# Kernel tuning notes

Hardware: AMD Instinct MI355X
Metric: run time of the kernel (lower is better)

## Reference

```python
import jax, jax.numpy as jnp
import numpy as np
from jax import lax

N = 16384      # total nodes (NG graphs x PER nodes)
PER = 512      # nodes per graph
NG = 32        # number of graphs
E = 262144     # edges (avg degree 16)
NEG = jnp.float32(-1e30)


def gcn_conv(x, W, b, src, dst, em, n):
    # PyG GCNConv: h = xW; add *remaining* self-loops; symmetric norm; aggregate at dst; + bias
    h = x @ W
    w = em.astype(x.dtype)
    selfw = jax.ops.segment_sum(jnp.where((src == dst) & em, 1.0, 0.0), dst, num_segments=n)
    has_self = (selfw > 0).astype(x.dtype)
    deg = jax.ops.segment_sum(w, dst, num_segments=n) + (1.0 - has_self)
    dinv = lax.rsqrt(deg)
    norm = dinv[src] * dinv[dst] * w                      # [E]
    agg = jax.ops.segment_sum(norm[:, None] * h[src], dst, num_segments=n)
    return agg + ((1.0 - has_self) / deg)[:, None] * h + b


def edge_pool(x, src, dst, em, nvalid, Pw, Pb, n):
    # PyG EdgePooling with softmax edge scores, add_to_edge_score=0.1, eval-mode dropout (identity)
    e = src.shape[0]
    raw = (jnp.concatenate([x[src], x[dst]], axis=1) @ Pw)[:, 0] + Pb[0]
    # softmax over edges grouped by target node
    logits = jnp.where(em, raw, NEG)
    mx = jax.ops.segment_max(logits, dst, num_segments=n)
    ex = jnp.where(em, jnp.exp(raw - mx[dst]), 0.0)
    den = jax.ops.segment_sum(ex, dst, num_segments=n)
    score = jnp.where(em, ex / jnp.maximum(den[dst], 1e-16), 0.0) + 0.1
    # greedy sequential edge contraction in descending score order (matches PyG __merge_edges__)
    key = lax.stop_gradient(jnp.where(em, score, NEG))
    order = jnp.argsort(-key)

    def step(marked, sdm):
        s, d, mk = sdm
        ok = mk & ~marked[s] & ~marked[d]
        m1 = marked.at[s].set(marked[s] | ok)
        m2 = m1.at[d].set(m1[d] | ok)
        return m2, ok

    _, ch_sorted = lax.scan(step, ~nvalid, (src[order], dst[order], em[order]))
    chosen = jnp.zeros(e, bool).at[order].set(ch_sorted)

    rep = jnp.minimum(src, dst)
    oth = jnp.maximum(src, dst)
    SEN = n  # out-of-range index -> dropped scatter
    cluster = jnp.arange(n, dtype=src.dtype).at[jnp.where(chosen, oth, SEN)].set(rep, mode='drop')
    node_score = jnp.ones(n, x.dtype).at[jnp.where(chosen, rep, SEN)].set(score, mode='drop')
    absorbed = jnp.zeros(n, bool).at[jnp.where(chosen & (src != dst), oth, SEN)].set(True, mode='drop')
    new_valid = nvalid & ~absorbed
    # new_x[c] = (sum of x over cluster) * edge score (1 for unmatched nodes)
    new_x = jax.ops.segment_sum(x, cluster, num_segments=n) * node_score[:, None]
    new_x = new_x * new_valid[:, None].astype(x.dtype)
    # remap + coalesce edges (dedupe); padding kept via mask
    ns, nd = cluster[src], cluster[dst]
    ekey = jnp.where(em, ns * n + nd, n * n)
    eo = jnp.argsort(ekey)
    ks = ekey[eo]
    dup = jnp.concatenate([jnp.zeros(1, bool), ks[1:] == ks[:-1]])
    return new_x, ns[eo], nd[eo], (ks < n * n) & ~dup, new_valid


def _forward(x, W1, b1, W2, b2, W3, b3, P1w, P1b, P2w, P2b, P3w, P3b,
             L1w, L1b, L2w, L2b, L3w, L3b, edge_index, batch):
    n = x.shape[0]
    src, dst = edge_index[0], edge_index[1]
    em = jnp.ones(src.shape[0], bool)
    nv = jnp.ones(n, bool)
    h = gcn_conv(x, W1, b1, src, dst, em, n)
    h, src, dst, em, nv = edge_pool(h, src, dst, em, nv, P1w, P1b, n)
    h = jax.nn.relu(h)
    h = gcn_conv(h, W2, b2, src, dst, em, n)
    h, src, dst, em, nv = edge_pool(h, src, dst, em, nv, P2w, P2b, n)
    h = jax.nn.relu(h)
    h = gcn_conv(h, W3, b3, src, dst, em, n)
    h, src, dst, em, nv = edge_pool(h, src, dst, em, nv, P3w, P3b, n)
    h = jax.nn.relu(h)
    beff = jnp.where(nv, batch, NG)                       # invalid nodes -> dummy segment
    g = jax.ops.segment_max(h, beff, num_segments=NG + 1)[:NG]
    z = jax.nn.relu(g @ L1w + L1b)
    z = jax.nn.relu(z @ L2w + L2b)
    z = jax.nn.relu(z @ L3w + L3b)
    return jax.nn.softmax(z, axis=-1)


def _lin(k, fi, fo):
    w = jax.random.normal(k, (fi, fo), jnp.float32) * (1.0 / np.sqrt(fi))
    return w, jnp.zeros((fo,), jnp.float32)


def setup_inputs() -> dict:
    key = jax.random.key(0)
    ks = jax.random.split(key, 16)
    x = jax.random.normal(ks[0], (N, 107), jnp.float32)
    src = jax.random.randint(ks[1], (E,), 0, N, dtype=jnp.int32)
    dst = (src // PER) * PER + jax.random.randint(ks[2], (E,), 0, PER, dtype=jnp.int32)
    edge_index = jnp.stack([src, dst])
    batch = jnp.arange(N, dtype=jnp.int32) // PER
    W1, b1 = _lin(ks[3], 107, 200)
    W2, b2 = _lin(ks[4], 200, 400)
    W3, b3 = _lin(ks[5], 400, 600)
    P1w, P1b = _lin(ks[6], 400, 1)
    P2w, P2b = _lin(ks[7], 800, 1)
    P3w, P3b = _lin(ks[8], 1200, 1)
    L1w, L1b = _lin(ks[9], 600, 200)
    L2w, L2b = _lin(ks[10], 200, 20)
    L3w, L3b = _lin(ks[11], 20, 4)
    return dict(x=x, edge_index=edge_index, batch=batch,
                W1=W1, b1=b1, W2=W2, b2=b2, W3=W3, b3=b3,
                P1w=P1w, P1b=P1b, P2w=P2w, P2b=P2b, P3w=P3w, P3b=P3b,
                L1w=L1w, L1b=L1b, L2w=L2w, L2b=L2b, L3w=L3w, L3b=L3b)


def reference(x, edge_index, batch, W1, b1, W2, b2, W3, b3,
              P1w, P1b, P2w, P2b, P3w, P3b, L1w, L1b, L2w, L2b, L3w, L3b):
    return _forward(x, W1, b1, W2, b2, W3, b3, P1w, P1b, P2w, P2b, P3w, P3b,
                    L1w, L1b, L2w, L2b, L3w, L3b, edge_index, batch)
```

## Files before the change

kernel.cpp:

```cpp
#include <hip/hip_runtime.h>

#define NN 16384
#define PERG 512
#define NGR 32
#define NE 262144
#define GSEG 9216

__device__ __forceinline__ unsigned encf(float f){
  unsigned u = __float_as_uint(f);
  return (u & 0x80000000u) ? ~u : (u | 0x80000000u);
}
__device__ __forceinline__ float decf(unsigned e){
  unsigned u = (e & 0x80000000u) ? (e ^ 0x80000000u) : ~e;
  return __uint_as_float(u);
}

__global__ void k_padx(const float* __restrict__ x, float* __restrict__ xp){
  int i = blockIdx.x*256 + threadIdx.x;
  if (i < NN*112){ int r = i/112, c = i-r*112; xp[i] = (c<107) ? x[r*107+c] : 0.f; }
}
__global__ void k_padw(const float* __restrict__ Wsrc, float* __restrict__ Wdst,
                       int Ksrc, int Kdst, int N){
  int i = blockIdx.x*256 + threadIdx.x;
  if (i < Kdst*N){ int r = i/N, c = i-r*N; Wdst[i] = (r<Ksrc) ? Wsrc[r*N+c] : 0.f; }
}

__global__ __launch_bounds__(256) void k_bucket(const int* __restrict__ ei, int* __restrict__ gcount,
    int* __restrict__ bsrc, int* __restrict__ bdst, int* __restrict__ bem, int* __restrict__ beid){
  __shared__ int cnt[NGR];
  __shared__ int base[NGR];
  int t = threadIdx.x;
  if (t < NGR) cnt[t] = 0;
  __syncthreads();
  int e = blockIdx.x*256 + t;
  int s=0,d=0,g=0,r=0;
  bool ok = (e < NE);
  if (ok){ s = ei[e]; d = ei[NE+e]; g = s >> 9; r = atomicAdd(&cnt[g],1); }
  __syncthreads();
  if (t < NGR) base[t] = atomicAdd(&gcount[t], cnt[t]);
  __syncthreads();
  if (ok){
    int pos = g*GSEG + base[g] + r;
    bsrc[pos]=s; bdst[pos]=d; bem[pos]=1; beid[pos]=e;
  }
}
__global__ void k_init_nodes(int* __restrict__ valid){
  int i = blockIdx.x*256 + threadIdx.x;
  if (i < NN) valid[i]=1;
}

__global__ __launch_bounds__(256) void k_mm(const float* __restrict__ A, const float* __restrict__ W,
                                            float* __restrict__ C, int KP, int N){
  __shared__ float As[16][132];
  __shared__ float Ws[16][68];
  int col0 = blockIdx.x*64, row0 = blockIdx.y*128;
  int t = threadIdx.x;
  int tx = t & 15, ty = t >> 4;
  int ar = t >> 1;
  int ak = (t & 1) * 8;
  int wk = t >> 4;
  int wn = (t & 15) * 4;
  int wc = col0 + wn;

  float acc[8][4];
#pragma unroll
  for (int i=0;i<8;i++)
#pragma unroll
    for (int j=0;j<4;j++) acc[i][j]=0.f;

  const float* Arow = A + (size_t)(row0+ar)*KP;

  for (int k0=0; k0<KP; k0+=16){
    float4 a0 = *(const float4*)&Arow[k0 + ak];
    float4 a1 = *(const float4*)&Arow[k0 + ak + 4];
    float4 w0;
    const float* wp = &W[(size_t)(k0+wk)*N + wc];
    if (wc+3 < N) w0 = *(const float4*)wp;
    else { w0.x=(wc<N)?wp[0]:0.f; w0.y=(wc+1<N)?wp[1]:0.f; w0.z=(wc+2<N)?wp[2]:0.f; w0.w=0.f; }
    __syncthreads();
    As[ak+0][ar]=a0.x; As[ak+1][ar]=a0.y; As[ak+2][ar]=a0.z; As[ak+3][ar]=a0.w;
    As[ak+4][ar]=a1.x; As[ak+5][ar]=a1.y; As[ak+6][ar]=a1.z; As[ak+7][ar]=a1.w;
    *(float4*)&Ws[wk][wn] = w0;
    __syncthreads();
#pragma unroll
    for (int kk=0;kk<16;kk++){
      float4 A0 = *(const float4*)&As[kk][ty*8];
      float4 A1 = *(const float4*)&As[kk][ty*8+4];
      float4 B0 = *(const float4*)&Ws[kk][tx*4];
      float a[8] = {A0.x,A0.y,A0.z,A0.w,A1.x,A1.y,A1.z,A1.w};
      float b[4] = {B0.x,B0.y,B0.z,B0.w};
#pragma unroll
      for (int i=0;i<8;i++)
#pragma unroll
        for (int j=0;j<4;j++) acc[i][j] += a[i]*b[j];
    }
  }

#pragma unroll
  for (int i=0;i<8;i++){
    int r = row0 + ty*8 + i;
    int cc = col0 + tx*4;
    if (cc+3 < N){
      float4 v = {acc[i][0],acc[i][1],acc[i][2],acc[i][3]};
      *(float4*)&C[(size_t)r*N+cc] = v;
    } else {
#pragma unroll
      for (int j=0;j<4;j++) if (cc+j<N) C[(size_t)r*N+cc+j] = acc[i][j];
    }
  }
}

__global__ __launch_bounds__(1024) void k_prep(const int* __restrict__ bsrc, const int* __restrict__ bdst,
    const int* __restrict__ bem, const int* __restrict__ gcount,
    int* __restrict__ row_s, int* __restrict__ row_e, int* __restrict__ elist,
    float* __restrict__ dinv, float* __restrict__ selfco){
  int g = blockIdx.x, t = threadIdx.x;
  __shared__ int cnt_l[PERG];
  __shared__ int scn[PERG];
  __shared__ int cur[PERG];
  __shared__ unsigned char hs_l[PERG];
  if (t<PERG){ cnt_l[t]=0; hs_l[t]=0; }
  __syncthreads();
  int nE = min(gcount[g], GSEG); int base = g*GSEG;
  for (int k=t;k<nE;k+=1024){
    if (bem[base+k]){
      int d = bdst[base+k]&511;
      atomicAdd(&cnt_l[d],1);
      if (bsrc[base+k]==bdst[base+k]) hs_l[d]=1;
    }
  }
  __syncthreads();
  if (t<PERG) scn[t]=cnt_l[t];
  __syncthreads();
  for (int off=1; off<PERG; off<<=1){
    int v = (t<PERG && t>=off) ? scn[t-off] : 0;
    __syncthreads();
    if (t<PERG) scn[t]+=v;
    __syncthreads();
  }
  if (t<PERG){
    int excl = scn[t]-cnt_l[t];
    row_s[g*PERG+t] = base+excl;
    row_e[g*PERG+t] = base+scn[t];
    cur[t] = excl;
    float deg = (float)cnt_l[t] + (hs_l[t]?0.f:1.f);
    dinv[g*PERG+t]   = rsqrtf(deg);
    selfco[g*PERG+t] = hs_l[t]?0.f:(1.f/deg);
  }
  __syncthreads();
  for (int k=t;k<nE;k+=1024){
    if (bem[base+k]){
      int d = bdst[base+k]&511;
      elist[base + atomicAdd(&cur[d],1)] = base+k;
    }
  }
}

template<int FO>
__global__ __launch_bounds__(256) void k_aggab(const float* __restrict__ h, const int* __restrict__ row_s,
    const int* __restrict__ row_e, const int* __restrict__ elist, const int* __restrict__ bsrc,
    const float* __restrict__ dinv, const float* __restrict__ selfco, const float* __restrict__ bias,
    const float* __restrict__ Pw, float* __restrict__ y, float* __restrict__ aval, float* __restrict__ bval){
  constexpr int Q = (FO+63)/64;
  int lane = threadIdx.x & 63;
  int nblk = (blockIdx.x & 7)*512 + (blockIdx.x >> 3);
  int i = nblk*4 + (threadIdx.x>>6);
  float acc[Q];
#pragma unroll
  for (int q=0;q<Q;q++) acc[q]=0.f;
  int s0 = row_s[i], s1 = row_e[i];
  float di = dinv[i];
  for (int p=s0; p<s1; p++){
    int e = elist[p]; int s = bsrc[e];
    float nr = di * dinv[s];
    const float* hrow = h + (size_t)s*FO;
#pragma unroll
    for (int q=0;q<Q;q++){ int c=lane+q*64; if (c<FO) acc[q] += nr*hrow[c]; }
  }
  float sc = selfco[i];
  const float* hi = h + (size_t)i*FO;
  float* yi = y + (size_t)i*FO;
  float sa=0.f, sb=0.f;
#pragma unroll
  for (int q=0;q<Q;q++){
    int c = lane+q*64;
    if (c<FO){
      float v = acc[q] + sc*hi[c] + bias[c];
      yi[c] = v;
      sa += v*Pw[c];
      sb += v*Pw[FO+c];
    }
  }
  for (int o=32;o;o>>=1){ sa += __shfl_xor(sa,o); sb += __shfl_xor(sb,o); }
  if (lane==0){ aval[i]=sa; bval[i]=sb; }
}

#define NEPT 9
__global__ __launch_bounds__(1024) void k_pool(const int* __restrict__ gcount,
    int* __restrict__ bsrc, int* __restrict__ bdst, int* __restrict__ bem, const int* __restrict__ beid,
    const float* __restrict__ aval, const float* __restrict__ bval, const float* __restrict__ Pb,
    float* __restrict__ nscore, int* __restrict__ partner, int* __restrict__ valid, int* __restrict__ table){
  int g = blockIdx.x, t = threadIdx.x;
  __shared__ unsigned mx[PERG];
  __shared__ float den[PERG];
  __shared__ unsigned long long best[PERG];
  __shared__ unsigned char marked[PERG];
  __shared__ unsigned short clus[PERG];
  __shared__ int flag;
  int nE = min(gcount[g], GSEG), base = g*GSEG;
  if (t<PERG){
    mx[t]=0u; den[t]=0.f;
    marked[t] = valid[g*PERG+t] ? 0 : 1;
    clus[t] = (unsigned short)t;
    nscore[g*PERG+t] = 1.f;
    partner[g*PERG+t] = -1;
  }
  __syncthreads();

  int sL[NEPT], dL[NEPT];
  float rawv[NEPT];
  unsigned em = 0u;
#pragma unroll
  for (int j=0;j<NEPT;j++){
    sL[j]=0; dL[j]=0; rawv[j]=0.f;
    int k = t + j*1024;
    if (k < nE && bem[base+k]){
      sL[j] = bsrc[base+k]&511; dL[j] = bdst[base+k]&511;
      rawv[j] = aval[(g<<9)+sL[j]] + bval[(g<<9)+dL[j]] + Pb[0];
      em |= (1u<<j);
      atomicMax(&mx[dL[j]], encf(rawv[j]));
    }
  }
  __syncthreads();
  float exv[NEPT];
#pragma unroll
  for (int j=0;j<NEPT;j++){
    exv[j]=0.f;
    if (em & (1u<<j)){
      exv[j] = expf(rawv[j] - decf(mx[dL[j]]));
      atomicAdd(&den[dL[j]], exv[j]);
    }
  }
  __syncthreads();
  unsigned long long pri[NEPT];
#pragma unroll
  for (int j=0;j<NEPT;j++){
    pri[j]=0ull;
    if (em & (1u<<j)){
      int k = t + j*1024;
      float sc = exv[j]/fmaxf(den[dL[j]],1e-16f) + 0.1f;
      pri[j] = ((unsigned long long)__float_as_uint(sc) << 18)
             | (unsigned long long)(0x3FFFFu - (unsigned)beid[base+k]);
    }
  }

  unsigned live = em;
  for (int round=0; round<512; ++round){
    if (t<PERG) best[t]=0ull;
    if (t==0) flag = 0;
    __syncthreads();
    int any = 0;
#pragma unroll
    for (int j=0;j<NEPT;j++){
      if (!(live & (1u<<j))) continue;
      int ls=sL[j], ld=dL[j];
      if (marked[ls] | marked[ld]){ live &= ~(1u<<j); continue; }
      any = 1;
      atomicMax(&best[ls], pri[j]);
      if (ld != ls) atomicMax(&best[ld], pri[j]);
    }
    if (any) flag = 1;
    __syncthreads();
    if (!flag) break;
#pragma unroll
    for (int j=0;j<NEPT;j++){
      if (!(live & (1u<<j))) continue;
      int ls=sL[j], ld=dL[j];
      unsigned long long p = pri[j];
      if (best[ls]==p && best[ld]==p){
        int repl = min(ls,ld), oth = max(ls,ld);
        clus[oth] = (unsigned short)repl;
        nscore[g*PERG+repl] = __uint_as_float((unsigned)(p>>18));
        if (ls != ld){ valid[g*PERG+oth] = 0; partner[g*PERG+repl] = g*PERG+oth; }
        marked[ls] = 1; marked[ld] = 1;
        live &= ~(1u<<j);
      }
    }
    __syncthreads();
  }
  __syncthreads();

#pragma unroll
  for (int j=0;j<NEPT;j++){
    if (em & (1u<<j)){
      int k = t + j*1024;
      int ns = clus[sL[j]], nd = clus[dL[j]];
      sL[j]=ns; dL[j]=nd;
      bsrc[base+k] = (g<<9)+ns; bdst[base+k] = (g<<9)+nd;
      table[(g<<18) | (ns<<9) | nd] = 0x7FFFFFFF;
    }
  }
  __syncthreads();
#pragma unroll
  for (int j=0;j<NEPT;j++){
    if (em & (1u<<j)){
      int k = t + j*1024;
      atomicMin(&table[(g<<18) | (sL[j]<<9) | dL[j]], base+k);
    }
  }
  __syncthreads();
#pragma unroll
  for (int j=0;j<NEPT;j++){
    if (em & (1u<<j)){
      int k = t + j*1024;
      if (table[(g<<18) | (sL[j]<<9) | dL[j]] != base+k) bem[base+k] = 0;
    }
  }
}

template<int FO, int FOP>
__global__ __launch_bounds__(256) void k_newx(const float* __restrict__ y, const int* __restrict__ partner,
    const float* __restrict__ nscore, const int* __restrict__ valid, float* __restrict__ out){
  constexpr int Q = (FOP+63)/64;
  int lane = threadIdx.x & 63;
  int nblk = (blockIdx.x & 7)*512 + (blockIdx.x >> 3);
  int i = nblk*4 + (threadIdx.x>>6);
  int v = valid[i];
  float ns = nscore[i];
  int p = partner[i];
  const float* yi = y + (size_t)i*FO;
  const float* yp = (p>=0) ? (y + (size_t)p*FO) : yi;
  float* oi = out + (size_t)i*FOP;
#pragma unroll
  for (int q=0;q<Q;q++){
    int c = lane + q*64;
    if (c<FO){
      float val = yi[c];
      if (p>=0) val += yp[c];
      val *= ns;
      oi[c] = v ? fmaxf(val,0.f) : 0.f;
    } else if (c<FOP){
      oi[c] = 0.f;
    }
  }
}

__global__ __launch_bounds__(256) void k_gmax(const float* __restrict__ x, const int* __restrict__ valid,
                                              float* __restrict__ part){
  int g = blockIdx.x >> 3, rp = blockIdx.x & 7;
  __shared__ int lv[64];
  int r0 = rp*64;
  if (threadIdx.x < 64) lv[threadIdx.x] = valid[g*PERG + r0 + threadIdx.x];
  __syncthreads();
  const float* base = x + ((size_t)g*PERG + r0)*600;
  for (int c=threadIdx.x; c<600; c+=256){
    float m = -1e30f;
    for (int r=0;r<64;r++)
      if (lv[r]) m = fmaxf(m, base[(size_t)r*600+c]);
    part[(size_t)(g*8+rp)*600 + c] = m;
  }
}
__global__ __launch_bounds__(256) void k_head(const float* __restrict__ part,
    const float* __restrict__ L1w, const float* __restrict__ L1b,
    const float* __restrict__ L2w, const float* __restrict__ L2b,
    const float* __restrict__ L3w, const float* __restrict__ L3b, float* __restrict__ out){
  int g = blockIdx.x, t = threadIdx.x;
  __shared__ float gg[600];
  __shared__ float z1[200];
  __shared__ float z2[20];
  __shared__ float z3[4];
  for (int c=t;c<600;c+=256){
    float m = -1e30f;
#pragma unroll
    for (int rp=0;rp<8;rp++) m = fmaxf(m, part[(size_t)(g*8+rp)*600 + c]);
    gg[c] = m;
  }
  __syncthreads();
  if (t<200){
    float s = L1b[t];
#pragma unroll 4
    for (int k=0;k<600;k++) s += gg[k]*L1w[k*200+t];
    z1[t] = fmaxf(s,0.f);
  }
  __syncthreads();
  if (t<20){
    float s = L2b[t];
#pragma unroll 4
    for (int k=0;k<200;k++) s += z1[k]*L2w[k*20+t];
    z2[t] = fmaxf(s,0.f);
  }
  __syncthreads();
  if (t<4){
    float s = L3b[t];
    for (int k=0;k<20;k++) s += z2[k]*L3w[k*4+t];
    z3[t] = fmaxf(s,0.f);
  }
  __syncthreads();
  if (t==0){
    float m = fmaxf(fmaxf(z3[0],z3[1]), fmaxf(z3[2],z3[3]));
    float e0=expf(z3[0]-m), e1=expf(z3[1]-m), e2=expf(z3[2]-m), e3=expf(z3[3]-m);
    float s = e0+e1+e2+e3;
    out[g*4+0]=e0/s; out[g*4+1]=e1/s; out[g*4+2]=e2/s; out[g*4+3]=e3/s;
  }
}

struct WsPtrs {
  float *A, *B, *x0p, *W1p, *W2p;
  int *bsrc, *bdst, *bem, *beid;
  int *elist, *row_s, *row_e;
  float *dinv, *selfco, *aval, *bval;
  float *nscore; int *partner; int *valid;
  int *gcount;
  float *gbuf;
};

extern "C" void kernel_launch(void* const* d_in, const int* in_sizes, int n_in,
                              void* d_out, int out_size, void* d_ws, size_t ws_size,
                              hipStream_t stream){
  const float* x0  = (const float*)d_in[0];
  const int*   ei  = (const int*)  d_in[1];
  const float* W1  = (const float*)d_in[3];  const float* b1  = (const float*)d_in[4];
  const float* W2  = (const float*)d_in[5];  const float* b2  = (const float*)d_in[6];
  const float* W3  = (const float*)d_in[7];  const float* b3  = (const float*)d_in[8];
  const float* P1w = (const float*)d_in[9];  const float* P1b = (const float*)d_in[10];
  const float* P2w = (const float*)d_in[11]; const float* P2b = (const float*)d_in[12];
  const float* P3w = (const float*)d_in[13]; const float* P3b = (const float*)d_in[14];
  const float* L1w = (const float*)d_in[15]; const float* L1b = (const float*)d_in[16];
  const float* L2w = (const float*)d_in[17]; const float* L2b = (const float*)d_in[18];
  const float* L3w = (const float*)d_in[19]; const float* L3b = (const float*)d_in[20];
  float* out = (float*)d_out;

  char* w = (char*)d_ws;
  size_t off = 0;
  auto alloc = [&](size_t bytes)->void*{
    void* p = w + off;
    off += bytes;
    off = (off + 255) & ~(size_t)255;
    return p;
  };
  WsPtrs P;
  P.A     = (float*)alloc((size_t)NN*600*4);
  P.B     = (float*)alloc((size_t)NN*600*4);
  P.x0p   = (float*)alloc((size_t)NN*112*4);
  P.W1p   = (float*)alloc((size_t)112*200*4);
  P.W2p   = (float*)alloc((size_t)208*400*4);
  P.bsrc  = (int*)  alloc((size_t)NGR*GSEG*4);
  P.bdst  = (int*)  alloc((size_t)NGR*GSEG*4);
  P.bem   = (int*)  alloc((size_t)NGR*GSEG*4);
  P.beid  = (int*)  alloc((size_t)NGR*GSEG*4);
  P.elist = (int*)  alloc((size_t)NGR*GSEG*4);
  P.row_s = (int*)  alloc((size_t)NN*4);
  P.row_e = (int*)  alloc((size_t)NN*4);
  P.dinv   = (float*)alloc((size_t)NN*4);
  P.selfco = (float*)alloc((size_t)NN*4);
  P.aval   = (float*)alloc((size_t)NN*4);
  P.bval   = (float*)alloc((size_t)NN*4);
  P.nscore = (float*)alloc((size_t)NN*4);
  P.partner= (int*)  alloc((size_t)NN*4);
  P.valid  = (int*)  alloc((size_t)NN*4);
  P.gcount = (int*)  alloc((size_t)NGR*4);
  P.gbuf   = (float*)alloc((size_t)NGR*8*600*4);
  (void)ws_size; (void)in_sizes; (void)n_in; (void)out_size;

  const int NG4 = NN/4;

  k_padx<<<(NN*112+255)/256,256,0,stream>>>(x0, P.x0p);
  k_padw<<<(112*200+255)/256,256,0,stream>>>(W1, P.W1p, 107, 112, 200);
  k_padw<<<(208*400+255)/256,256,0,stream>>>(W2, P.W2p, 200, 208, 400);
  hipMemsetAsync(P.gcount, 0, NGR*sizeof(int), stream);
  k_bucket<<<NE/256,256,0,stream>>>(ei, P.gcount, P.bsrc, P.bdst, P.bem, P.beid);
  k_init_nodes<<<NN/256,256,0,stream>>>(P.valid);

  { dim3 gmm(4,128); k_mm<<<gmm,256,0,stream>>>(P.x0p, P.W1p, P.A, 112, 200); }
  k_prep<<<NGR,1024,0,stream>>>(P.bsrc,P.bdst,P.bem,P.gcount,P.row_s,P.row_e,P.elist,P.dinv,P.selfco);
  k_aggab<200><<<NG4,256,0,stream>>>(P.A,P.row_s,P.row_e,P.elist,P.bsrc,P.dinv,P.selfco,b1,P1w,P.B,P.aval,P.bval);
  k_pool<<<NGR,1024,0,stream>>>(P.gcount,P.bsrc,P.bdst,P.bem,P.beid,P.aval,P.bval,P1b,
                                P.nscore,P.partner,P.valid,(int*)P.A);
  k_newx<200,208><<<NG4,256,0,stream>>>(P.B,P.partner,P.nscore,P.valid,P.A);

  { dim3 gmm(7,128); k_mm<<<gmm,256,0,stream>>>(P.A, P.W2p, P.B, 208, 400); }
  k_prep<<<NGR,1024,0,stream>>>(P.bsrc,P.bdst,P.bem,P.gcount,P.row_s,P.row_e,P.elist,P.dinv,P.selfco);
  k_aggab<400><<<NG4,256,0,stream>>>(P.B,P.row_s,P.row_e,P.elist,P.bsrc,P.dinv,P.selfco,b2,P2w,P.A,P.aval,P.bval);
  k_pool<<<NGR,1024,0,stream>>>(P.gcount,P.bsrc,P.bdst,P.bem,P.beid,P.aval,P.bval,P2b,
                                P.nscore,P.partner,P.valid,(int*)P.B);
  k_newx<400,400><<<NG4,256,0,stream>>>(P.A,P.partner,P.nscore,P.valid,P.B);

  { dim3 gmm(10,128); k_mm<<<gmm,256,0,stream>>>(P.B, W3, P.A, 400, 600); }
  k_prep<<<NGR,1024,0,stream>>>(P.bsrc,P.bdst,P.bem,P.gcount,P.row_s,P.row_e,P.elist,P.dinv,P.selfco);
  k_aggab<600><<<NG4,256,0,stream>>>(P.A,P.row_s,P.row_e,P.elist,P.bsrc,P.dinv,P.selfco,b3,P3w,P.B,P.aval,P.bval);
  k_pool<<<NGR,1024,0,stream>>>(P.gcount,P.bsrc,P.bdst,P.bem,P.beid,P.aval,P.bval,P3b,
                                P.nscore,P.partner,P.valid,(int*)P.A);
  k_newx<600,600><<<NG4,256,0,stream>>>(P.B,P.partner,P.nscore,P.valid,P.A);

  k_gmax<<<NGR*8,256,0,stream>>>(P.A, P.valid, P.gbuf);
  k_head<<<NGR,256,0,stream>>>(P.gbuf, L1w, L1b, L2w, L2b, L3w, L3b, out);
}
```

Baseline: 988.2 us.

## Replace edge-parallel greedy matching rounds with node-centric incidence-list scans

Builds a per-graph node incidence CSR (both endpoints) in k_prep and rewrites the k_pool matching loop so each unmarked node scans its incident edges for the best unmarked neighbour, instead of every edge doing 64-bit atomicMax on shared per-node best values each round. Scores go into shared memory and ties are broken by loading edge ids from global memory. This removes shared atomics and the wide priority keys, but it adds a second prefix scan and CSR build in k_prep. It also uses only 512 of 1024 threads per round with serial per-node loops, and raises the round cap to 600.

```diff
diff --git a/kernel.cpp b/kernel.cpp
--- a/kernel.cpp
+++ b/kernel.cpp
@@ -113,20 +113,25 @@
 __global__ __launch_bounds__(1024) void k_prep(const int* __restrict__ bsrc, const int* __restrict__ bdst,
     const int* __restrict__ bem, const int* __restrict__ gcount,
     int* __restrict__ row_s, int* __restrict__ row_e, int* __restrict__ elist,
+    int* __restrict__ inc, int* __restrict__ inc_rs, int* __restrict__ inc_re,
     float* __restrict__ dinv, float* __restrict__ selfco){
   int g = blockIdx.x, t = threadIdx.x;
   __shared__ int cnt_l[PERG];
+  __shared__ int cnt2[PERG];
   __shared__ int scn[PERG];
   __shared__ int cur[PERG];
+  __shared__ int cur2[PERG];
   __shared__ unsigned char hs_l[PERG];
-  if (t<PERG){ cnt_l[t]=0; hs_l[t]=0; }
-  __syncthreads();
-  int nE = min(gcount[g], GSEG); int base = g*GSEG;
+  if (t<PERG){ cnt_l[t]=0; cnt2[t]=0; hs_l[t]=0; }
+  __syncthreads();
+  int nE = min(gcount[g], GSEG); int base = g*GSEG; int base2 = g*2*GSEG;
   for (int k=t;k<nE;k+=1024){
     if (bem[base+k]){
-      int d = bdst[base+k]&511;
+      int d = bdst[base+k]&511, s = bsrc[base+k]&511;
       atomicAdd(&cnt_l[d],1);
-      if (bsrc[base+k]==bdst[base+k]) hs_l[d]=1;
+      if (s==d) hs_l[d]=1;
+      atomicAdd(&cnt2[d],1);
+      atomicAdd(&cnt2[s],1);
     }
   }
   __syncthreads();
@@ -148,10 +153,27 @@
     selfco[g*PERG+t] = hs_l[t]?0.f:(1.f/deg);
   }
   __syncthreads();
+  if (t<PERG) scn[t]=cnt2[t];
+  __syncthreads();
+  for (int off=1; off<PERG; off<<=1){
+    int v = (t<PERG && t>=off) ? scn[t-off] : 0;
+    __syncthreads();
+    if (t<PERG) scn[t]+=v;
+    __syncthreads();
+  }
+  if (t<PERG){
+    int excl = scn[t]-cnt2[t];
+    inc_rs[g*PERG+t] = base2+excl;
+    inc_re[g*PERG+t] = base2+scn[t];
+    cur2[t] = excl;
+  }
+  __syncthreads();
   for (int k=t;k<nE;k+=1024){
     if (bem[base+k]){
-      int d = bdst[base+k]&511;
+      int d = bdst[base+k]&511, s = bsrc[base+k]&511;
       elist[base + atomicAdd(&cur[d],1)] = base+k;
+      inc[base2 + atomicAdd(&cur2[d],1)] = (s<<14)|k;
+      inc[base2 + atomicAdd(&cur2[s],1)] = (d<<14)|k;
     }
   }
 }
@@ -198,22 +220,25 @@
 #define NEPT 9
 __global__ __launch_bounds__(1024) void k_pool(const int* __restrict__ gcount,
     int* __restrict__ bsrc, int* __restrict__ bdst, int* __restrict__ bem, const int* __restrict__ beid,
+    const int* __restrict__ inc, const int* __restrict__ inc_rs, const int* __restrict__ inc_re,
     const float* __restrict__ aval, const float* __restrict__ bval, const float* __restrict__ Pb,
     float* __restrict__ nscore, int* __restrict__ partner, int* __restrict__ valid, int* __restrict__ table){
   int g = blockIdx.x, t = threadIdx.x;
+  __shared__ unsigned sbl[GSEG];
   __shared__ unsigned mx[PERG];
   __shared__ float den[PERG];
-  __shared__ unsigned long long best[PERG];
   __shared__ unsigned char marked[PERG];
   __shared__ unsigned short clus[PERG];
+  __shared__ unsigned short best_e[PERG];
+  __shared__ unsigned short best_o[PERG];
   __shared__ int flag;
   int nE = min(gcount[g], GSEG), base = g*GSEG;
   if (t<PERG){
     mx[t]=0u; den[t]=0.f;
-    marked[t] = valid[g*PERG+t] ? 0 : 1;
+    marked[t] = valid[(g<<9)+t] ? 0 : 1;
     clus[t] = (unsigned short)t;
-    nscore[g*PERG+t] = 1.f;
-    partner[g*PERG+t] = -1;
+    nscore[(g<<9)+t] = 1.f;
+    partner[(g<<9)+t] = -1;
   }
   __syncthreads();
 
@@ -242,48 +267,56 @@
     }
   }
   __syncthreads();
-  unsigned long long pri[NEPT];
 #pragma unroll
   for (int j=0;j<NEPT;j++){
-    pri[j]=0ull;
     if (em & (1u<<j)){
       int k = t + j*1024;
       float sc = exv[j]/fmaxf(den[dL[j]],1e-16f) + 0.1f;
-      pri[j] = ((unsigned long long)__float_as_uint(sc) << 18)
-             | (unsigned long long)(0x3FFFFu - (unsigned)beid[base+k]);
-    }
-  }
-
-  unsigned live = em;
-  for (int round=0; round<512; ++round){
-    if (t<PERG) best[t]=0ull;
+      sbl[k] = __float_as_uint(sc);
+    }
+  }
+  __syncthreads();
+
+  for (int round=0; round<600; ++round){
+    if (t<PERG){ best_e[t]=0xFFFF; best_o[t]=0xFFFF; }
     if (t==0) flag = 0;
     __syncthreads();
-    int any = 0;
-#pragma unroll
-    for (int j=0;j<NEPT;j++){
-      if (!(live & (1u<<j))) continue;
-      int ls=sL[j], ld=dL[j];
-      if (marked[ls] | marked[ld]){ live &= ~(1u<<j); continue; }
-      any = 1;
-      atomicMax(&best[ls], pri[j]);
-      if (ld != ls) atomicMax(&best[ld], pri[j]);
-    }
-    if (any) flag = 1;
+    if (t<PERG && !marked[t]){
+      int n = t;
+      unsigned bsb = 0u; int bk = -1, bo = 0; unsigned bbe = 0xFFFFFFFFu;
+      int j1 = inc_re[(g<<9)+n];
+      for (int j=inc_rs[(g<<9)+n]; j<j1; j++){
+        unsigned en = (unsigned)inc[j];
+        int o = en>>14, k_ = en & 0x3FFF;
+        if (marked[o]) continue;
+        unsigned sv = sbl[k_];
+        if (sv < bsb) continue;
+        if (sv > bsb){ bsb=sv; bk=k_; bo=o; bbe=0xFFFFFFFFu; }
+        else {
+          if (bbe==0xFFFFFFFFu) bbe = (unsigned)beid[base+bk];
+          unsigned nb = (unsigned)beid[base+k_];
+          if (nb < bbe){ bk=k_; bo=o; bbe=nb; }
+        }
+      }
+      if (bk>=0){ best_e[n]=(unsigned short)bk; best_o[n]=(unsigned short)bo; flag=1; }
+    }
     __syncthreads();
     if (!flag) break;
-#pragma unroll
-    for (int j=0;j<NEPT;j++){
-      if (!(live & (1u<<j))) continue;
-      int ls=sL[j], ld=dL[j];
-      unsigned long long p = pri[j];
-      if (best[ls]==p && best[ld]==p){
-        int repl = min(ls,ld), oth = max(ls,ld);
-        clus[oth] = (unsigned short)repl;
-        nscore[g*PERG+repl] = __uint_as_float((unsigned)(p>>18));
-        if (ls != ld){ valid[g*PERG+oth] = 0; partner[g*PERG+repl] = g*PERG+oth; }
-        marked[ls] = 1; marked[ld] = 1;
-        live &= ~(1u<<j);
+    if (t<PERG && !marked[t]){
+      int n = t;
+      int bk = best_e[n];
+      if (bk != 0xFFFF){
+        int o = best_o[n];
+        if (o == n){
+          nscore[(g<<9)+n] = __uint_as_float(sbl[bk]);
+          marked[n] = 1;
+        } else if (best_e[o]==bk && n<o){
+          clus[o] = (unsigned short)n;
+          nscore[(g<<9)+n] = __uint_as_float(sbl[bk]);
+          valid[(g<<9)+o] = 0;
+          partner[(g<<9)+n] = (g<<9)+o;
+          marked[n] = 1; marked[o] = 1;
+        }
       }
     }
     __syncthreads();
@@ -408,6 +441,7 @@
   float *A, *B, *x0p, *W1p, *W2p;
   int *bsrc, *bdst, *bem, *beid;
   int *elist, *row_s, *row_e;
+  int *inc, *inc_rs, *inc_re;
   float *dinv, *selfco, *aval, *bval;
   float *nscore; int *partner; int *valid;
   int *gcount;
@@ -449,6 +483,9 @@
   P.bem   = (int*)  alloc((size_t)NGR*GSEG*4);
   P.beid  = (int*)  alloc((size_t)NGR*GSEG*4);
   P.elist = (int*)  alloc((size_t)NGR*GSEG*4);
+  P.inc   = (int*)  alloc((size_t)NGR*2*GSEG*4);
+  P.inc_rs= (int*)  alloc((size_t)NN*4);
+  P.inc_re= (int*)  alloc((size_t)NN*4);
   P.row_s = (int*)  alloc((size_t)NN*4);
   P.row_e = (int*)  alloc((size_t)NN*4);
   P.dinv   = (float*)alloc((size_t)NN*4);
@@ -472,24 +509,27 @@
   k_init_nodes<<<NN/256,256,0,stream>>>(P.valid);
 
   { dim3 gmm(4,128); k_mm<<<gmm,256,0,stream>>>(P.x0p, P.W1p, P.A, 112, 200); }
-  k_prep<<<NGR,1024,0,stream>>>(P.bsrc,P.bdst,P.bem,P.gcount,P.row_s,P.row_e,P.elist,P.dinv,P.selfco);
+  k_prep<<<NGR,1024,0,stream>>>(P.bsrc,P.bdst,P.bem,P.gcount,P.row_s,P.row_e,P.elist,
+                                P.inc,P.inc_rs,P.inc_re,P.dinv,P.selfco);
   k_aggab<200><<<NG4,256,0,stream>>>(P.A,P.row_s,P.row_e,P.elist,P.bsrc,P.dinv,P.selfco,b1,P1w,P.B,P.aval,P.bval);
-  k_pool<<<NGR,1024,0,stream>>>(P.gcount,P.bsrc,P.bdst,P.bem,P.beid,P.aval,P.bval,P1b,
-                                P.nscore,P.partner,P.valid,(int*)P.A);
+  k_pool<<<NGR,1024,0,stream>>>(P.gcount,P.bsrc,P.bdst,P.bem,P.beid,P.inc,P.inc_rs,P.inc_re,
+                                P.aval,P.bval,P1b,P.nscore,P.partner,P.valid,(int*)P.A);
   k_newx<200,208><<<NG4,256,0,stream>>>(P.B,P.partner,P.nscore,P.valid,P.A);
 
   { dim3 gmm(7,128); k_mm<<<gmm,256,0,stream>>>(P.A, P.W2p, P.B, 208, 400); }
-  k_prep<<<NGR,1024,0,stream>>>(P.bsrc,P.bdst,P.bem,P.gcount,P.row_s,P.row_e,P.elist,P.dinv,P.selfco);
+  k_prep<<<NGR,1024,0,stream>>>(P.bsrc,P.bdst,P.bem,P.gcount,P.row_s,P.row_e,P.elist,
+                                P.inc,P.inc_rs,P.inc_re,P.dinv,P.selfco);
   k_aggab<400><<<NG4,256,0,stream>>>(P.B,P.row_s,P.row_e,P.elist,P.bsrc,P.dinv,P.selfco,b2,P2w,P.A,P.aval,P.bval);
-  k_pool<<<NGR,1024,0,stream>>>(P.gcount,P.bsrc,P.bdst,P.bem,P.beid,P.aval,P.bval,P2b,
-                                P.nscore,P.partner,P.valid,(int*)P.B);
+  k_pool<<<NGR,1024,0,stream>>>(P.gcount,P.bsrc,P.bdst,P.bem,P.beid,P.inc,P.inc_rs,P.inc_re,
+                                P.aval,P.bval,P2b,P.nscore,P.partner,P.valid,(int*)P.B);
   k_newx<400,400><<<NG4,256,0,stream>>>(P.A,P.partner,P.nscore,P.valid,P.B);
 
   { dim3 gmm(10,128); k_mm<<<gmm,256,0,stream>>>(P.B, W3, P.A, 400, 600); }
-  k_prep<<<NGR,1024,0,stream>>>(P.bsrc,P.bdst,P.bem,P.gcount,P.row_s,P.row_e,P.elist,P.dinv,P.selfco);
+  k_prep<<<NGR,1024,0,stream>>>(P.bsrc,P.bdst,P.bem,P.gcount,P.row_s,P.row_e,P.elist,
+                                P.inc,P.inc_rs,P.inc_re,P.dinv,P.selfco);
   k_aggab<600><<<NG4,256,0,stream>>>(P.A,P.row_s,P.row_e,P.elist,P.bsrc,P.dinv,P.selfco,b3,P3w,P.B,P.aval,P.bval);
-  k_pool<<<NGR,1024,0,stream>>>(P.gcount,P.bsrc,P.bdst,P.bem,P.beid,P.aval,P.bval,P3b,
-                                P.nscore,P.partner,P.valid,(int*)P.A);
+  k_pool<<<NGR,1024,0,stream>>>(P.gcount,P.bsrc,P.bdst,P.bem,P.beid,P.inc,P.inc_rs,P.inc_re,
+                                P.aval,P.bval,P3b,P.nscore,P.partner,P.valid,(int*)P.A);
   k_newx<600,600><<<NG4,256,0,stream>>>(P.B,P.partner,P.nscore,P.valid,P.A);
 
   k_gmax<<<NGR*8,256,0,stream>>>(P.A, P.valid, P.gbuf);
```

Result: slower. 2.469 ms (+149.9%).

## Replace iterative matching rounds with LDS bitonic sort and single-wave greedy scan

Applied to the files above, without the earlier changes.

The pooling kernel's repeated rounds of atomicMax locally-dominant matching are replaced by a bitonic sort of packed edge keys (score, edge-id tiebreak, index) in dynamic LDS, followed by one wavefront that walks the sorted list in 64-edge chunks and resolves conflicts with ballots and shuffles. This mirrors the reference greedy order directly and drops the up-to-512 barrier-separated rounds, at the cost of a full 16K-element sort with many barriers and a serial single-wave scan. Separately, the CSR edge list now stores source node ids directly, which removes one indirection per edge in aggregation.

```diff
diff --git a/kernel.cpp b/kernel.cpp
--- a/kernel.cpp
+++ b/kernel.cpp
@@ -5,6 +5,9 @@
 #define NGR 32
 #define NE 262144
 #define GSEG 9216
+#define NSORT 16384
+
+typedef unsigned long long u64;
 
 __device__ __forceinline__ unsigned encf(float f){
   unsigned u = __float_as_uint(f);
@@ -151,14 +154,14 @@
   for (int k=t;k<nE;k+=1024){
     if (bem[base+k]){
       int d = bdst[base+k]&511;
-      elist[base + atomicAdd(&cur[d],1)] = base+k;
+      elist[base + atomicAdd(&cur[d],1)] = bsrc[base+k];
     }
   }
 }
 
 template<int FO>
 __global__ __launch_bounds__(256) void k_aggab(const float* __restrict__ h, const int* __restrict__ row_s,
-    const int* __restrict__ row_e, const int* __restrict__ elist, const int* __restrict__ bsrc,
+    const int* __restrict__ row_e, const int* __restrict__ elist,
     const float* __restrict__ dinv, const float* __restrict__ selfco, const float* __restrict__ bias,
     const float* __restrict__ Pw, float* __restrict__ y, float* __restrict__ aval, float* __restrict__ bval){
   constexpr int Q = (FO+63)/64;
@@ -171,7 +174,7 @@
   int s0 = row_s[i], s1 = row_e[i];
   float di = dinv[i];
   for (int p=s0; p<s1; p++){
-    int e = elist[p]; int s = bsrc[e];
+    int s = elist[p];
     float nr = di * dinv[s];
     const float* hrow = h + (size_t)s*FO;
 #pragma unroll
@@ -200,21 +203,22 @@
     int* __restrict__ bsrc, int* __restrict__ bdst, int* __restrict__ bem, const int* __restrict__ beid,
     const float* __restrict__ aval, const float* __restrict__ bval, const float* __restrict__ Pb,
     float* __restrict__ nscore, int* __restrict__ partner, int* __restrict__ valid, int* __restrict__ table){
-  int g = blockIdx.x, t = threadIdx.x;
+  extern __shared__ u64 skL[];
   __shared__ unsigned mx[PERG];
   __shared__ float den[PERG];
-  __shared__ unsigned long long best[PERG];
   __shared__ unsigned char marked[PERG];
   __shared__ unsigned short clus[PERG];
-  __shared__ int flag;
+  int g = blockIdx.x, t = threadIdx.x;
   int nE = min(gcount[g], GSEG), base = g*GSEG;
   if (t<PERG){
     mx[t]=0u; den[t]=0.f;
-    marked[t] = valid[g*PERG+t] ? 0 : 1;
+    marked[t] = valid[(g<<9)+t] ? 0 : 1;
     clus[t] = (unsigned short)t;
-    nscore[g*PERG+t] = 1.f;
-    partner[g*PERG+t] = -1;
-  }
+    nscore[(g<<9)+t] = 1.f;
+    partner[(g<<9)+t] = -1;
+  }
+#pragma unroll
+  for (int q=0;q<NSORT/1024;q++) skL[t + q*1024] = 0ull;
   __syncthreads();
 
   int sL[NEPT], dL[NEPT];
@@ -242,51 +246,76 @@
     }
   }
   __syncthreads();
-  unsigned long long pri[NEPT];
 #pragma unroll
   for (int j=0;j<NEPT;j++){
-    pri[j]=0ull;
     if (em & (1u<<j)){
       int k = t + j*1024;
       float sc = exv[j]/fmaxf(den[dL[j]],1e-16f) + 0.1f;
-      pri[j] = ((unsigned long long)__float_as_uint(sc) << 18)
-             | (unsigned long long)(0x3FFFFu - (unsigned)beid[base+k]);
-    }
-  }
-
-  unsigned live = em;
-  for (int round=0; round<512; ++round){
-    if (t<PERG) best[t]=0ull;
-    if (t==0) flag = 0;
-    __syncthreads();
-    int any = 0;
-#pragma unroll
-    for (int j=0;j<NEPT;j++){
-      if (!(live & (1u<<j))) continue;
-      int ls=sL[j], ld=dL[j];
-      if (marked[ls] | marked[ld]){ live &= ~(1u<<j); continue; }
-      any = 1;
-      atomicMax(&best[ls], pri[j]);
-      if (ld != ls) atomicMax(&best[ld], pri[j]);
-    }
-    if (any) flag = 1;
-    __syncthreads();
-    if (!flag) break;
-#pragma unroll
-    for (int j=0;j<NEPT;j++){
-      if (!(live & (1u<<j))) continue;
-      int ls=sL[j], ld=dL[j];
-      unsigned long long p = pri[j];
-      if (best[ls]==p && best[ld]==p){
-        int repl = min(ls,ld), oth = max(ls,ld);
-        clus[oth] = (unsigned short)repl;
-        nscore[g*PERG+repl] = __uint_as_float((unsigned)(p>>18));
-        if (ls != ld){ valid[g*PERG+oth] = 0; partner[g*PERG+repl] = g*PERG+oth; }
-        marked[ls] = 1; marked[ld] = 1;
-        live &= ~(1u<<j);
+      u64 inv = (u64)(0x3FFFFu - (unsigned)beid[base+k]);
+      skL[k] = ((u64)__float_as_uint(sc) << 32) | (inv << 14) | (u64)k;
+    }
+  }
+
+  for (unsigned ksz=2; ksz<=NSORT; ksz<<=1){
+    for (unsigned jsz=ksz>>1; jsz>0; jsz>>=1){
+      __syncthreads();
+#pragma unroll 1
+      for (int i=t; i<NSORT; i+=1024){
+        int jj = i ^ (int)jsz;
+        if (jj > i){
+          bool up = ((i & (int)ksz) == 0);
+          u64 x = skL[i], y = skL[jj];
+          if (up ? (x < y) : (x > y)){ skL[i]=y; skL[jj]=x; }
+        }
       }
     }
-    __syncthreads();
+  }
+  __syncthreads();
+
+#pragma unroll
+  for (int q=0;q<NSORT/1024;q++){
+    int i = t + q*1024;
+    u64 key = skL[i];
+    if (key){
+      int k_ = (int)(key & 0x3FFFu);
+      u64 sv = key >> 32;
+      u64 s_ = (u64)(bsrc[base+k_]&511), d_ = (u64)(bdst[base+k_]&511);
+      skL[i] = (sv<<32) | (s_<<23) | (d_<<14);
+    }
+  }
+  __syncthreads();
+
+  if (t < 64){
+    int lane = t;
+    for (int c0=0; c0<NSORT; c0+=64){
+      u64 rec = skL[c0 + lane];
+      unsigned long long anyb = __ballot(rec != 0ull);
+      if (anyb == 0ull) break;
+      int s = (int)((rec>>23)&511), d = (int)((rec>>14)&511);
+      unsigned sb = (unsigned)(rec>>32);
+      bool live = (rec!=0ull) && !marked[s] && !marked[d];
+      unsigned long long pend = __ballot(live);
+      while (pend){
+        int first = __builtin_ctzll(pend);
+        int sf = __shfl(s, first), df = __shfl(d, first);
+        if (lane == first){
+          if (s == d){
+            marked[s] = 1;
+            nscore[(g<<9)+s] = __uint_as_float(sb);
+          } else {
+            int rep = min(s,d), oth = max(s,d);
+            clus[oth] = (unsigned short)rep;
+            nscore[(g<<9)+rep] = __uint_as_float(sb);
+            valid[(g<<9)+oth] = 0;
+            partner[(g<<9)+rep] = (g<<9)+oth;
+            marked[s] = 1; marked[d] = 1;
+          }
+        }
+        pend &= ~(1ull<<first);
+        bool die = (s==sf || s==df || d==sf || d==df);
+        pend &= ~__ballot(die);
+      }
+    }
   }
   __syncthreads();
 
@@ -463,6 +492,7 @@
   (void)ws_size; (void)in_sizes; (void)n_in; (void)out_size;
 
   const int NG4 = NN/4;
+  const int POOL_LDS = NSORT * 8;
 
   k_padx<<<(NN*112+255)/256,256,0,stream>>>(x0, P.x0p);
   k_padw<<<(112*200+255)/256,256,0,stream>>>(W1, P.W1p, 107, 112, 200);
@@ -473,23 +503,23 @@
 
   { dim3 gmm(4,128); k_mm<<<gmm,256,0,stream>>>(P.x0p, P.W1p, P.A, 112, 200); }
   k_prep<<<NGR,1024,0,stream>>>(P.bsrc,P.bdst,P.bem,P.gcount,P.row_s,P.row_e,P.elist,P.dinv,P.selfco);
-  k_aggab<200><<<NG4,256,0,stream>>>(P.A,P.row_s,P.row_e,P.elist,P.bsrc,P.dinv,P.selfco,b1,P1w,P.B,P.aval,P.bval);
-  k_pool<<<NGR,1024,0,stream>>>(P.gcount,P.bsrc,P.bdst,P.bem,P.beid,P.aval,P.bval,P1b,
-                                P.nscore,P.partner,P.valid,(int*)P.A);
+  k_aggab<200><<<NG4,256,0,stream>>>(P.A,P.row_s,P.row_e,P.elist,P.dinv,P.selfco,b1,P1w,P.B,P.aval,P.bval);
+  k_pool<<<NGR,1024,POOL_LDS,stream>>>(P.gcount,P.bsrc,P.bdst,P.bem,P.beid,
+                                P.aval,P.bval,P1b,P.nscore,P.partner,P.valid,(int*)P.A);
   k_newx<200,208><<<NG4,256,0,stream>>>(P.B,P.partner,P.nscore,P.valid,P.A);
 
   { dim3 gmm(7,128); k_mm<<<gmm,256,0,stream>>>(P.A, P.W2p, P.B, 208, 400); }
   k_prep<<<NGR,1024,0,stream>>>(P.bsrc,P.bdst,P.bem,P.gcount,P.row_s,P.row_e,P.elist,P.dinv,P.selfco);
-  k_aggab<400><<<NG4,256,0,stream>>>(P.B,P.row_s,P.row_e,P.elist,P.bsrc,P.dinv,P.selfco,b2,P2w,P.A,P.aval,P.bval);
-  k_pool<<<NGR,1024,0,stream>>>(P.gcount,P.bsrc,P.bdst,P.bem,P.beid,P.aval,P.bval,P2b,
-                                P.nscore,P.partner,P.valid,(int*)P.B);
+  k_aggab<400><<<NG4,256,0,stream>>>(P.B,P.row_s,P.row_e,P.elist,P.dinv,P.selfco,b2,P2w,P.A,P.aval,P.bval);
+  k_pool<<<NGR,1024,POOL_LDS,stream>>>(P.gcount,P.bsrc,P.bdst,P.bem,P.beid,
+                                P.aval,P.bval,P2b,P.nscore,P.partner,P.valid,(int*)P.B);
   k_newx<400,400><<<NG4,256,0,stream>>>(P.A,P.partner,P.nscore,P.valid,P.B);
 
   { dim3 gmm(10,128); k_mm<<<gmm,256,0,stream>>>(P.B, W3, P.A, 400, 600); }
   k_prep<<<NGR,1024,0,stream>>>(P.bsrc,P.bdst,P.bem,P.gcount,P.row_s,P.row_e,P.elist,P.dinv,P.selfco);
-  k_aggab<600><<<NG4,256,0,stream>>>(P.A,P.row_s,P.row_e,P.elist,P.bsrc,P.dinv,P.selfco,b3,P3w,P.B,P.aval,P.bval);
-  k_pool<<<NGR,1024,0,stream>>>(P.gcount,P.bsrc,P.bdst,P.bem,P.beid,P.aval,P.bval,P3b,
-                                P.nscore,P.partner,P.valid,(int*)P.A);
+  k_aggab<600><<<NG4,256,0,stream>>>(P.A,P.row_s,P.row_e,P.elist,P.dinv,P.selfco,b3,P3w,P.B,P.aval,P.bval);
+  k_pool<<<NGR,1024,POOL_LDS,stream>>>(P.gcount,P.bsrc,P.bdst,P.bem,P.beid,
+                                P.aval,P.bval,P3b,P.nscore,P.partner,P.valid,(int*)P.A);
   k_newx<600,600><<<NG4,256,0,stream>>>(P.B,P.partner,P.nscore,P.valid,P.A);
 
   k_gmax<<<NGR*8,256,0,stream>>>(P.A, P.valid, P.gbuf);
```

Result: slower. 1.683 ms (+70.3%).
